# Kernel optimization log

Hardware: AMD Instinct MI355X
Metric: run time of the kernel (lower is better)

The kernel has to match this reference:

```python
import jax, jax.numpy as jnp
import numpy as np

B, L, DIN = 2, 4096, 1024
W = 64            # windowsize
G, H = 8, 8       # groups, heads per group
DQ = DV = 64
FF = 1024
NEG = -1e30


def rmsnorm(x, gamma, d):
    # F.normalize(x, dim=-1) * sqrt(d) * gamma
    n = jnp.sqrt(jnp.sum(x * x, axis=-1, keepdims=True))
    return x / jnp.maximum(n, 1e-12) * (d ** 0.5) * gamma


def setup_inputs() -> dict:
    key = jax.random.key(0)
    ks = jax.random.split(key, 8)
    s = 0.02
    return {
        "x": jax.random.normal(ks[0], (B, L, DIN), jnp.float32),
        "norm_gamma": jnp.ones((DIN,), jnp.float32),
        "Wq_w": jax.random.normal(ks[1], (G * H * DQ, DIN), jnp.float32) * s,
        "Wq_b": jnp.zeros((G * H * DQ,), jnp.float32),
        "Wkv_w": jax.random.normal(ks[2], (G * (DQ + DV), DIN), jnp.float32) * s,
        "Wkv_b": jnp.zeros((G * (DQ + DV),), jnp.float32),
        "wz_gamma1": jnp.ones((G * H * DV,), jnp.float32),
        "W1_w": jax.random.normal(ks[3], (2 * FF, G * H * DV), jnp.float32) * s,
        "W1_b": jnp.zeros((2 * FF,), jnp.float32),
        "wz_gamma2": jnp.ones((2 * FF,), jnp.float32),
        "W2_w": jax.random.normal(ks[4], (FF, 2 * FF), jnp.float32) * s,
        "W2_b": jnp.zeros((FF,), jnp.float32),
    }


def reference(x, norm_gamma, Wq_w, Wq_b, Wkv_w, Wkv_b,
              wz_gamma1, W1_w, W1_b, wz_gamma2, W2_w, W2_b):
    w2, w4 = W // 2, W // 4
    S = 2 * L // W  # number of query chunks (L % W == 0 -> drop_last path)

    xn = rmsnorm(x, norm_gamma, DIN)
    q = xn @ Wq_w.T + Wq_b          # [B, L, G*H*DQ]
    kv = xn @ Wkv_w.T + Wkv_b       # [B, L, G*(DQ+DV)]

    # pad_to_multiple(kv, W, mod=W//2): L % W == 0 -> append W//2 zeros
    kv = jnp.pad(kv, ((0, 0), (0, w2), (0, 0)))
    k, v = jnp.split(kv, 2, axis=-1)  # each [B, L+W/2, G*DQ]
    # F.pad W//4 both sides, then overlapping windows of size W, stride W//2
    k = jnp.pad(k, ((0, 0), (w4, w4), (0, 0)))  # [B, L+W, G*DQ]
    v = jnp.pad(v, ((0, 0), (w4, w4), (0, 0)))
    idx = jnp.arange(S)[:, None] * w2 + jnp.arange(W)[None, :]  # [S, W] (drop_last applied)
    kwin = k[:, idx].reshape(B, S, W, G, DQ).transpose(0, 3, 1, 2, 4)  # [B,G,S,W,DQ]
    vwin = v[:, idx].reshape(B, S, W, G, DV).transpose(0, 3, 1, 2, 4)  # [B,G,S,W,DV]

    # 'B (S w) (G H D) -> B G H S w D'
    qh = q.reshape(B, S, w2, G, H, DQ).transpose(0, 3, 4, 1, 2, 5)  # [B,G,H,S,w2,DQ]

    qk = jnp.einsum('bghsqd,bgskd->bghsqk', qh, kwin) * (1.0 / DQ ** 0.5)
    # edge masking: first chunk can't see left pad, last chunk can't see right pad
    maskb = jnp.zeros((S, W), bool).at[0, :w4].set(True).at[S - 1, W - w4:].set(True)
    qk = jnp.where(maskb[None, None, None, :, None, :], NEG, qk)
    attn = jax.nn.softmax(qk, axis=-1)
    o = jnp.einsum('bghsqk,bgskd->bghsqd', attn, vwin)
    o = o.transpose(0, 3, 4, 1, 2, 5).reshape(B, L, G * H * DV)  # 'B G H S w D -> B (S w) (G H D)'

    # Wz: RMSNorm -> Linear -> SiLU -> RMSNorm -> Linear -> SiLU (dropout=0)
    z = rmsnorm(o, wz_gamma1, G * H * DV)
    z = jax.nn.silu(z @ W1_w.T + W1_b)
    z = rmsnorm(z, wz_gamma2, 2 * FF)
    z = jax.nn.silu(z @ W2_w.T + W2_b)
    return z
```

## Files before the change

kernel.cpp:

```cpp
#include <hip/hip_runtime.h>
#include <cstdint>

typedef _Float16 f16;
typedef f16 f16x4 __attribute__((ext_vector_type(4)));
typedef f16 f16x8 __attribute__((ext_vector_type(8)));
typedef float f32x4 __attribute__((ext_vector_type(4)));

#define MFMA16(a, b, c) __builtin_amdgcn_mfma_f32_16x16x32_f16(a, b, c, 0, 0, 0)

static __device__ __forceinline__ void gload16(const void* g, void* l) {
    __builtin_amdgcn_global_load_lds(
        (const __attribute__((address_space(1))) uint32_t*)g,
        (__attribute__((address_space(3))) uint32_t*)l, 16, 0, 0);
}

template <int NM, int ND, int NV>
static __device__ __forceinline__ void sgb_phase() {
    if (NV > 0) __builtin_amdgcn_sched_group_barrier(0x10, NV, 0);
    constexpr int PER = NM / ND;
#pragma unroll
    for (int i = 0; i < ND; ++i) {
        __builtin_amdgcn_sched_group_barrier(0x8, PER, 0);
        __builtin_amdgcn_sched_group_barrier(0x100, 1, 0);
    }
    if (NM - PER * ND > 0)
        __builtin_amdgcn_sched_group_barrier(0x8, NM - PER * ND, 0);
}

static __device__ __forceinline__ float blockReduceSum256(float v) {
    __shared__ float red[4];
#pragma unroll
    for (int off = 32; off > 0; off >>= 1) v += __shfl_xor(v, off);
    if ((threadIdx.x & 63) == 0) red[threadIdx.x >> 6] = v;
    __syncthreads();
    return red[0] + red[1] + red[2] + red[3];
}

__global__ __launch_bounds__(256) void k_rmsnorm_x(const float* __restrict__ x,
                                                   const float* __restrict__ gamma,
                                                   f16* __restrict__ out) {
    size_t row = blockIdx.x;
    const float4 v = reinterpret_cast<const float4*>(x + row * 1024)[threadIdx.x];
    float ss = v.x * v.x + v.y * v.y + v.z * v.z + v.w * v.w;
    ss = blockReduceSum256(ss);
    float sc = 32.0f / fmaxf(sqrtf(ss), 1e-12f);
    const float4 g = reinterpret_cast<const float4*>(gamma)[threadIdx.x];
    f16x4 o;
    o[0] = (f16)(v.x * sc * g.x); o[1] = (f16)(v.y * sc * g.y);
    o[2] = (f16)(v.z * sc * g.z); o[3] = (f16)(v.w * sc * g.w);
    *reinterpret_cast<f16x4*>(out + row * 1024 + threadIdx.x * 4) = o;
}

__global__ __launch_bounds__(256) void k_prep(
    const float* __restrict__ Wq_w, const float* __restrict__ Wkv_w,
    const float* __restrict__ W1_w, const float* __restrict__ g1,
    const float* __restrict__ W2_w, const float* __restrict__ g2,
    const float* __restrict__ Wq_b, const float* __restrict__ Wkv_b,
    f16* __restrict__ wqkv, f16* __restrict__ w1, f16* __restrict__ w2,
    float* __restrict__ cb, float* __restrict__ scz) {
    int i = blockIdx.x * 256 + threadIdx.x;
    if (i < 1048576) {
        float4 v = reinterpret_cast<const float4*>(Wq_w)[i];
        f16x4 o; o[0] = (f16)v.x; o[1] = (f16)v.y; o[2] = (f16)v.z; o[3] = (f16)v.w;
        *reinterpret_cast<f16x4*>(wqkv + (size_t)i * 4) = o;
    } else if (i < 1310720) {
        int j = i - 1048576;
        float4 v = reinterpret_cast<const float4*>(Wkv_w)[j];
        f16x4 o; o[0] = (f16)v.x; o[1] = (f16)v.y; o[2] = (f16)v.z; o[3] = (f16)v.w;
        *reinterpret_cast<f16x4*>(wqkv + 4194304 + (size_t)j * 4) = o;
    } else if (i < 3407872) {
        int j = i - 1310720;
        float4 v = reinterpret_cast<const float4*>(W1_w)[j];
        int c = (j * 4) & 4095;
        f16x4 o;
        o[0] = (f16)(v.x * g1[c]);     o[1] = (f16)(v.y * g1[c + 1]);
        o[2] = (f16)(v.z * g1[c + 2]); o[3] = (f16)(v.w * g1[c + 3]);
        *reinterpret_cast<f16x4*>(w1 + (size_t)j * 4) = o;
    } else if (i < 3932160) {
        int j = i - 3407872;
        float4 v = reinterpret_cast<const float4*>(W2_w)[j];
        int c = (j * 4) & 2047;
        f16x4 o;
        o[0] = (f16)(v.x * g2[c]);     o[1] = (f16)(v.y * g2[c + 1]);
        o[2] = (f16)(v.z * g2[c + 2]); o[3] = (f16)(v.w * g2[c + 3]);
        *reinterpret_cast<f16x4*>(w2 + (size_t)j * 4) = o;
    } else if (i < 3933440) {
        int j = i - 3932160;
        int e = j * 4;
        float4 o4 = (e < 4096) ? reinterpret_cast<const float4*>(Wq_b)[j]
                               : reinterpret_cast<const float4*>(Wkv_b)[(e - 4096) >> 2];
        reinterpret_cast<float4*>(cb)[j] = o4;
    } else if (i < 3937536) {
        int j = i - 3933440;
        reinterpret_cast<float4*>(scz)[j] = make_float4(0.f, 0.f, 0.f, 0.f);
    }
}

template <int BN, int EPI, int MODE>
__global__ __launch_bounds__(512, 2) void k_gemm8p(const f16* __restrict__ A,
                                                   const f16* __restrict__ Bt,
                                                   const float* __restrict__ bias,
                                                   const float* __restrict__ ssin,
                                                   float sqrtD,
                                                   float* __restrict__ ssout,
                                                   void* __restrict__ Cout,
                                                   int M, int N, int K) {
    constexpr int BM = 256;
    constexpr int WN = BN / 64, WM = 8 / WN, WR = BM / WM;
    constexpr int MW = WR / 16, MH = MW / 2;
    constexpr int LA = 2, LB = BN / 128;
    constexpr int VS = 2 * LA + LB;
    constexpr int AK = BM * 32;
    constexpr int BKE = BN * 32;
    constexpr int SE = 2 * AK + 2 * BKE;

    __shared__ alignas(16) f16 lds[2 * SE];

    const int nb = N / BN;
    int bn, bm;
    if (MODE == 0) { bn = blockIdx.x & 7; bm = blockIdx.x >> 3; }
    else           { bn = blockIdx.x % nb; bm = blockIdx.x / nb; }

    const int tid = threadIdx.x, w = tid >> 6, l = tid & 63;
    const int wm = w / WN, wn = w % WN;
    const int lrow = l & 15, lq = l >> 4;
    const int g = (lrow >> 1) & 3;

    const f16* Ab = A + (size_t)bm * BM * K;
    const f16* Bb = Bt + (size_t)bn * BN * K;
    const int NT = K >> 6;

    int aoff[MW], boff[4];
#pragma unroll
    for (int m = 0; m < MW; ++m)
        aoff[m] = (wm * WR + m * 16 + lrow) * 32 + 8 * (lq ^ g);
#pragma unroll
    for (int n = 0; n < 4; ++n)
        boff[n] = (wn * 64 + n * 16 + lrow) * 32 + 8 * (lq ^ g);

    auto stageA = [&](int k0, f16* region) {
#pragma unroll
        for (int q = 0; q < LA; ++q) {
            int r = q * 128 + w * 16 + (l >> 2);
            int c = 8 * ((l & 3) ^ ((r >> 1) & 3));
            gload16(Ab + (size_t)r * K + k0 + c, region + q * 4096 + w * 512);
        }
    };
    auto stageB = [&](int k0, f16* region) {
#pragma unroll
        for (int q = 0; q < LB; ++q) {
            int r = q * 128 + w * 16 + (l >> 2);
            int c = 8 * ((l & 3) ^ ((r >> 1) & 3));
            gload16(Bb + (size_t)r * K + k0 + c, region + q * 4096 + w * 512);
        }
    };
    auto rdA = [&](f16x8 (&d)[MH], const f16* base, int h) {
#pragma unroll
        for (int m = 0; m < MH; ++m)
            d[m] = *reinterpret_cast<const f16x8*>(base + aoff[h * MH + m]);
    };
    auto rdB = [&](f16x8 (&d)[4], const f16* base) {
#pragma unroll
        for (int n = 0; n < 4; ++n)
            d[n] = *reinterpret_cast<const f16x8*>(base + boff[n]);
    };

    f32x4 acc[MW][4] = {};
    f16x8 afA[MH], afB[MH], bfA[4], bfB[4];

    auto mfmaLo = [&](f16x8 (&af)[MH], f16x8 (&bf)[4]) {
#pragma unroll
        for (int m = 0; m < MH; ++m)
#pragma unroll
            for (int n = 0; n < 4; ++n)
                acc[m][n] = MFMA16(af[m], bf[n], acc[m][n]);
    };
    auto mfmaHi = [&](f16x8 (&af)[MH], f16x8 (&bf)[4]) {
#pragma unroll
        for (int m = 0; m < MH; ++m)
#pragma unroll
            for (int n = 0; n < 4; ++n)
                acc[MH + m][n] = MFMA16(af[m], bf[n], acc[MH + m][n]);
    };

    stageA(0, lds);             stageB(0, lds + 2 * AK);
    stageA(32, lds + AK);       stageB(32, lds + 2 * AK + BKE);
    stageA(64, lds + SE);       stageB(64, lds + SE + 2 * AK);
    asm volatile("s_waitcnt vmcnt(%0)" :: "i"(2 * (LA + LB)) : "memory");
    __builtin_amdgcn_s_barrier();
    rdA(afA, lds, 0);
    rdB(bfA, lds + 2 * AK);

    const int NTm2 = NT - 2;
    for (int t = 0; t < NTm2; ++t) {
        f16* s0 = lds + (t & 1) * SE;
        f16* s1 = lds + ((t & 1) ^ 1) * SE;
        const int kn1 = (t + 1) << 6;
        const int kn2 = (t + 2) << 6;
        __builtin_amdgcn_s_barrier();
        stageA(kn1 + 32, s1 + AK);
        rdA(afB, s0, 1);
        mfmaLo(afA, bfA);
        sgb_phase<MH * 4, MH, LA>();
        asm volatile("s_waitcnt vmcnt(%0)" :: "i"(VS) : "memory");
        __builtin_amdgcn_s_barrier();
        stageB(kn1 + 32, s1 + 2 * AK + BKE);
        rdA(afA, s0 + AK, 0);
        rdB(bfB, s0 + 2 * AK + BKE);
        mfmaHi(afB, bfA);
        sgb_phase<MH * 4, MH + 4, LB>();
        __builtin_amdgcn_s_barrier();
        stageA(kn2, s0);
        rdA(afB, s0 + AK, 1);
        mfmaLo(afA, bfB);
        sgb_phase<MH * 4, MH, LA>();
        asm volatile("s_waitcnt vmcnt(%0)" :: "i"(VS) : "memory");
        __builtin_amdgcn_s_barrier();
        stageB(kn2, s0 + 2 * AK);
        rdA(afA, s1, 0);
        rdB(bfA, s1 + 2 * AK);
        mfmaHi(afB, bfB);
        sgb_phase<MH * 4, MH + 4, LB>();
    }
    {
        const int t = NTm2;
        f16* s0 = lds + (t & 1) * SE;
        f16* s1 = lds + ((t & 1) ^ 1) * SE;
        const int kn1 = (t + 1) << 6;
        __builtin_amdgcn_s_barrier();
        stageA(kn1 + 32, s1 + AK);
        rdA(afB, s0, 1);
        mfmaLo(afA, bfA);
        sgb_phase<MH * 4, MH, LA>();
        asm volatile("s_waitcnt vmcnt(%0)" :: "i"(VS) : "memory");
        __builtin_amdgcn_s_barrier();
        stageB(kn1 + 32, s1 + 2 * AK + BKE);
        rdA(afA, s0 + AK, 0);
        rdB(bfB, s0 + 2 * AK + BKE);
        mfmaHi(afB, bfA);
        sgb_phase<MH * 4, MH + 4, LB>();
        __builtin_amdgcn_s_barrier();
        rdA(afB, s0 + AK, 1);
        mfmaLo(afA, bfB);
        sgb_phase<MH * 4, MH, 0>();
        asm volatile("s_waitcnt vmcnt(%0)" :: "i"(LA + LB) : "memory");
        __builtin_amdgcn_s_barrier();
        rdA(afA, s1, 0);
        rdB(bfA, s1 + 2 * AK);
        mfmaHi(afB, bfB);
        sgb_phase<MH * 4, MH + 4, 0>();
    }
    {
        f16* s0 = lds + ((NT - 1) & 1) * SE;
        __builtin_amdgcn_s_barrier();
        rdA(afB, s0, 1);
        mfmaLo(afA, bfA);
        sgb_phase<MH * 4, MH, 0>();
        asm volatile("s_waitcnt vmcnt(0)" ::: "memory");
        __builtin_amdgcn_s_barrier();
        rdA(afA, s0 + AK, 0);
        rdB(bfB, s0 + 2 * AK + BKE);
        mfmaHi(afB, bfA);
        sgb_phase<MH * 4, MH + 4, 0>();
        __builtin_amdgcn_s_barrier();
        rdA(afB, s0 + AK, 1);
        mfmaLo(afA, bfB);
        sgb_phase<MH * 4, MH, 0>();
        mfmaHi(afB, bfB);
    }

    const size_t row0 = (size_t)bm * BM + wm * WR;
    const int col0 = bn * BN + wn * 64;
    float bsv[4];
#pragma unroll
    for (int n = 0; n < 4; ++n) bsv[n] = bias[col0 + n * 16 + lrow];
#pragma unroll
    for (int m = 0; m < MW; ++m) {
#pragma unroll
        for (int r = 0; r < 4; ++r) {
            const size_t row = row0 + m * 16 + lq * 4 + r;
            float scl = 1.0f;
            if (EPI >= 1)
                scl = sqrtD / fmaxf(sqrtf(ssin[row]), 1e-12f);
            float ssp = 0.f;
#pragma unroll
            for (int n = 0; n < 4; ++n) {
                float v = acc[m][n][r];
                if (EPI >= 1) v = v * scl;
                v += bsv[n];
                if (EPI >= 1) v = v / (1.f + __expf(-v));
                if (EPI == 1) ssp += v * v;
                const size_t idx = row * N + col0 + n * 16 + lrow;
                if (EPI == 2) reinterpret_cast<float*>(Cout)[idx] = v;
                else          reinterpret_cast<f16*>(Cout)[idx] = (f16)v;
            }
            if (EPI == 1) {
                ssp += __shfl_xor(ssp, 1);
                ssp += __shfl_xor(ssp, 2);
                ssp += __shfl_xor(ssp, 4);
                ssp += __shfl_xor(ssp, 8);
                if (lrow == 0) atomicAdd(&ssout[row], ssp);
            }
        }
    }
}

__global__ __launch_bounds__(256) void k_attn(const f16* __restrict__ qkv,
                                              f16* __restrict__ o,
                                              float* __restrict__ ssout) {
    __shared__ alignas(16) f16 Ksm[64 * 64];
    __shared__ alignas(16) f16 Vtsm[64 * 64];
    __shared__ alignas(16) f16 Psm[4][64 * 64];
    const int idx = blockIdx.x;
    const int s = idx & 127;
    const int g = (idx >> 7) & 7;
    const int b = idx >> 10;
    const int tid = threadIdx.x;
    const int w = tid >> 6, l = tid & 63;

    const int baseR = s * 32 - 16;
#pragma unroll
    for (int i = 0; i < 2; ++i) {
        const int j = i * 32 + (tid >> 3);
        const int d0 = (tid & 7) * 8;
        const int R = baseR + j;
        f16x8 kvv = {}, vvv = {};
        if (R >= 0 && R < 4096) {
            const f16* rp = qkv + ((size_t)(b * 4096 + R)) * 5120 + 4096 + g * 64 + d0;
            kvv = *reinterpret_cast<const f16x8*>(rp);
            vvv = *reinterpret_cast<const f16x8*>(rp + 512);
        }
        *reinterpret_cast<f16x8*>(&Ksm[j * 64 + d0]) = kvv;
#pragma unroll
        for (int e = 0; e < 8; ++e) Vtsm[(d0 + e) * 64 + j] = vvv[e];
    }

    const int lrow = l & 15, lk = (l >> 4) * 8;
    f16x8 aq[4][2];
#pragma unroll
    for (int m = 0; m < 4; ++m) {
        const int qr = w * 64 + m * 16 + lrow;
        const int h = qr >> 5, qi = qr & 31;
        const f16* qp = qkv + ((size_t)(b * 4096 + s * 32 + qi)) * 5120 + (g * 8 + h) * 64 + lk;
        aq[m][0] = *reinterpret_cast<const f16x8*>(qp);
        aq[m][1] = *reinterpret_cast<const f16x8*>(qp + 32);
    }
    __syncthreads();

    f32x4 acc[4][4] = {};
#pragma unroll
    for (int kk = 0; kk < 2; ++kk) {
        f16x8 bk[4];
#pragma unroll
        for (int n = 0; n < 4; ++n)
            bk[n] = *reinterpret_cast<const f16x8*>(&Ksm[(n * 16 + lrow) * 64 + kk * 32 + lk]);
#pragma unroll
        for (int m = 0; m < 4; ++m)
#pragma unroll
            for (int n = 0; n < 4; ++n)
                acc[m][n] = MFMA16(aq[m][kk], bk[n], acc[m][n]);
    }

    const int nlo = (s == 0) ? 1 : 0;
    const int nhi = (s == 127) ? 3 : 4;
#pragma unroll
    for (int m = 0; m < 4; ++m) {
#pragma unroll
        for (int r = 0; r < 4; ++r) {
            float xv[4];
#pragma unroll
            for (int n = 0; n < 4; ++n) xv[n] = acc[m][n][r] * 0.125f;
            float mx = -1e30f;
            for (int n = nlo; n < nhi; ++n) mx = fmaxf(mx, xv[n]);
#pragma unroll
            for (int off = 8; off > 0; off >>= 1) mx = fmaxf(mx, __shfl_xor(mx, off));
            float pv[4]; float sum = 0.f;
#pragma unroll
            for (int n = 0; n < 4; ++n) {
                float e = (n >= nlo && n < nhi) ? __expf(xv[n] - mx) : 0.f;
                pv[n] = e; sum += e;
            }
#pragma unroll
            for (int off = 8; off > 0; off >>= 1) sum += __shfl_xor(sum, off);
            const float inv = 1.f / sum;
            const int prow = m * 16 + (l >> 4) * 4 + r;
#pragma unroll
            for (int n = 0; n < 4; ++n)
                Psm[w][prow * 64 + n * 16 + lrow] = (f16)(pv[n] * inv);
        }
    }
    __syncthreads();

    f32x4 oacc[4][4] = {};
#pragma unroll
    for (int kk = 0; kk < 2; ++kk) {
        f16x8 ap[4], bv[4];
#pragma unroll
        for (int m = 0; m < 4; ++m)
            ap[m] = *reinterpret_cast<const f16x8*>(&Psm[w][(m * 16 + lrow) * 64 + kk * 32 + lk]);
#pragma unroll
        for (int n = 0; n < 4; ++n)
            bv[n] = *reinterpret_cast<const f16x8*>(&Vtsm[(n * 16 + lrow) * 64 + kk * 32 + lk]);
#pragma unroll
        for (int m = 0; m < 4; ++m)
#pragma unroll
            for (int n = 0; n < 4; ++n)
                oacc[m][n] = MFMA16(ap[m], bv[n], oacc[m][n]);
    }
    const int lr4 = (l >> 4) * 4;
#pragma unroll
    for (int m = 0; m < 4; ++m) {
#pragma unroll
        for (int r = 0; r < 4; ++r) {
            const int qr = w * 64 + m * 16 + lr4 + r;
            const int h = qr >> 5, qi = qr & 31;
            f16* op = o + ((size_t)(b * 4096 + s * 32 + qi)) * 4096 + (g * 8 + h) * 64;
            float ssp = 0.f;
#pragma unroll
            for (int n = 0; n < 4; ++n) {
                float v = oacc[m][n][r];
                op[n * 16 + lrow] = (f16)v;
                ssp += v * v;
            }
            ssp += __shfl_xor(ssp, 1);
            ssp += __shfl_xor(ssp, 2);
            ssp += __shfl_xor(ssp, 4);
            ssp += __shfl_xor(ssp, 8);
            if (lrow == 0)
                atomicAdd(&ssout[(size_t)(b * 4096 + s * 32 + qi)], ssp);
        }
    }
}

extern "C" void kernel_launch(void* const* d_in, const int* in_sizes, int n_in,
                              void* d_out, int out_size, void* d_ws, size_t ws_size,
                              hipStream_t stream) {
    const float* x     = (const float*)d_in[0];
    const float* ng    = (const float*)d_in[1];
    const float* Wq_w  = (const float*)d_in[2];
    const float* Wq_b  = (const float*)d_in[3];
    const float* Wkv_w = (const float*)d_in[4];
    const float* Wkv_b = (const float*)d_in[5];
    const float* g1    = (const float*)d_in[6];
    const float* W1_w  = (const float*)d_in[7];
    const float* W1_b  = (const float*)d_in[8];
    const float* g2    = (const float*)d_in[9];
    const float* W2_w  = (const float*)d_in[10];
    const float* W2_b  = (const float*)d_in[11];
    float* out = (float*)d_out;

    char* p = (char*)d_ws;
    f16* qkv  = (f16*)(p);
    f16* h1   = (f16*)(p);
    f16* xn   = (f16*)(p + 83886080);
    f16* ob   = (f16*)(p + 83886080);
    f16* w1   = (f16*)(p + 150994944);
    f16* w2   = (f16*)(p + 167772160);
    f16* wqkv = (f16*)(p + 171966464);
    float* cb  = (float*)(p + 182452224);
    float* sc1 = (float*)(p + 182472704);
    float* sc2 = (float*)(p + 182505472);

    k_prep<<<15381, 256, 0, stream>>>(Wq_w, Wkv_w, W1_w, g1, W2_w, g2, Wq_b, Wkv_b,
                                      wqkv, w1, w2, cb, sc1);
    k_rmsnorm_x<<<8192, 256, 0, stream>>>(x, ng, xn);

    k_gemm8p<256, 0, 1><<<640, 512, 0, stream>>>(xn, wqkv, cb, nullptr, 0.f, nullptr,
                                                 qkv, 8192, 5120, 1024);

    k_attn<<<2048, 256, 0, stream>>>(qkv, ob, sc1);

    k_gemm8p<256, 1, 0><<<256, 512, 0, stream>>>(ob, w1, W1_b, sc1, 64.0f, sc2,
                                                 h1, 8192, 2048, 4096);
    k_gemm8p<128, 2, 0><<<256, 512, 0, stream>>>(h1, w2, W2_b, sc2, 45.254834f, nullptr,
                                                 (void*)out, 8192, 1024, 2048);

    (void)in_sizes; (void)n_in; (void)out_size; (void)ws_size;
}
```

Before: 370.2 us.

## Switch GEMMs to 32x32x16 MFMA with XCD-aware tiling and separate row-norm pass

Replaces the 16x16x32 MFMA GEMM with a 32x32x16 variant that reads both A and B fragments per half-K step and uses wider accumulator tiles. It also adds an XCD-aware block-to-tile mapping so that blocks on the same XCD share A rows. The atomic sum-of-squares in the W1 epilogue is dropped, and a separate row reduction kernel over h1 now produces the norms for the W2 GEMM. The aim is higher MFMA throughput and fewer LDS reads per flop, at the cost of an extra launch that rereads h1 and higher register pressure.

Result: no change. 366.7 us (-1.0%).

```diff
diff --git a/kernel.cpp b/kernel.cpp
--- a/kernel.cpp
+++ b/kernel.cpp
@@ -5,8 +5,10 @@
 typedef f16 f16x4 __attribute__((ext_vector_type(4)));
 typedef f16 f16x8 __attribute__((ext_vector_type(8)));
 typedef float f32x4 __attribute__((ext_vector_type(4)));
+typedef float f32x16 __attribute__((ext_vector_type(16)));
 
 #define MFMA16(a, b, c) __builtin_amdgcn_mfma_f32_16x16x32_f16(a, b, c, 0, 0, 0)
+#define MFMA32(a, b, c) __builtin_amdgcn_mfma_f32_32x32x16_f16(a, b, c, 0, 0, 0)
 
 static __device__ __forceinline__ void gload16(const void* g, void* l) {
     __builtin_amdgcn_global_load_lds(
@@ -49,6 +51,24 @@
     o[0] = (f16)(v.x * sc * g.x); o[1] = (f16)(v.y * sc * g.y);
     o[2] = (f16)(v.z * sc * g.z); o[3] = (f16)(v.w * sc * g.w);
     *reinterpret_cast<f16x4*>(out + row * 1024 + threadIdx.x * 4) = o;
+}
+
+template <int D>
+__global__ __launch_bounds__(256) void k_rowss(const f16* __restrict__ in,
+                                               float* __restrict__ sc) {
+    constexpr int PER = D / 256;
+    size_t row = blockIdx.x;
+    const f16* ir = in + row * D;
+    int c0 = threadIdx.x * PER;
+    float ss = 0.f;
+#pragma unroll
+    for (int i = 0; i < PER; i += 8) {
+        f16x8 h = *reinterpret_cast<const f16x8*>(ir + c0 + i);
+#pragma unroll
+        for (int e = 0; e < 8; ++e) { float f = (float)h[e]; ss += f * f; }
+    }
+    ss = blockReduceSum256(ss);
+    if (threadIdx.x == 0) sc[row] = ss;
 }
 
 __global__ __launch_bounds__(256) void k_prep(
@@ -96,47 +116,55 @@
     }
 }
 
-template <int BN, int EPI, int MODE>
-__global__ __launch_bounds__(512, 2) void k_gemm8p(const f16* __restrict__ A,
+template <int BN, int EPI>
+__global__ __launch_bounds__(512, 2) void k_gemm32(const f16* __restrict__ A,
                                                    const f16* __restrict__ Bt,
                                                    const float* __restrict__ bias,
                                                    const float* __restrict__ ssin,
                                                    float sqrtD,
-                                                   float* __restrict__ ssout,
                                                    void* __restrict__ Cout,
                                                    int M, int N, int K) {
     constexpr int BM = 256;
-    constexpr int WN = BN / 64, WM = 8 / WN, WR = BM / WM;
-    constexpr int MW = WR / 16, MH = MW / 2;
+    constexpr int WN = BN / 64, WM = 8 / WN;
+    constexpr int WR = BM / WM, WC = BN / WN;
+    constexpr int MA = WR / 32, NB = WC / 32;
     constexpr int LA = 2, LB = BN / 128;
     constexpr int VS = 2 * LA + LB;
-    constexpr int AK = BM * 32;
-    constexpr int BKE = BN * 32;
+    constexpr int AK = BM * 32, BKE = BN * 32;
     constexpr int SE = 2 * AK + 2 * BKE;
 
     __shared__ alignas(16) f16 lds[2 * SE];
 
-    const int nb = N / BN;
-    int bn, bm;
-    if (MODE == 0) { bn = blockIdx.x & 7; bm = blockIdx.x >> 3; }
-    else           { bn = blockIdx.x % nb; bm = blockIdx.x / nb; }
+    const int mb = M / BM;
+    const int cpx = mb >> 3;
+    const int xcd = blockIdx.x & 7;
+    const int j = blockIdx.x >> 3;
+    const int bm = xcd * cpx + (j % cpx);
+    const int bn = j / cpx;
 
     const int tid = threadIdx.x, w = tid >> 6, l = tid & 63;
     const int wm = w / WN, wn = w % WN;
-    const int lrow = l & 15, lq = l >> 4;
-    const int g = (lrow >> 1) & 3;
+    const int cl = l & 31, h = l >> 5;
 
     const f16* Ab = A + (size_t)bm * BM * K;
     const f16* Bb = Bt + (size_t)bn * BN * K;
     const int NT = K >> 6;
 
-    int aoff[MW], boff[4];
-#pragma unroll
-    for (int m = 0; m < MW; ++m)
-        aoff[m] = (wm * WR + m * 16 + lrow) * 32 + 8 * (lq ^ g);
-#pragma unroll
-    for (int n = 0; n < 4; ++n)
-        boff[n] = (wn * 64 + n * 16 + lrow) * 32 + 8 * (lq ^ g);
+    int aoff[MA][2], boff[NB][2];
+#pragma unroll
+    for (int m = 0; m < MA; ++m) {
+        int r = wm * WR + m * 32 + cl;
+        int gg = (r >> 1) & 3;
+        aoff[m][0] = r * 32 + 8 * (h ^ gg);
+        aoff[m][1] = r * 32 + 8 * ((2 | h) ^ gg);
+    }
+#pragma unroll
+    for (int n = 0; n < NB; ++n) {
+        int r = wn * WC + n * 32 + cl;
+        int gg = (r >> 1) & 3;
+        boff[n][0] = r * 32 + 8 * (h ^ gg);
+        boff[n][1] = r * 32 + 8 * ((2 | h) ^ gg);
+    }
 
     auto stageA = [&](int k0, f16* region) {
 #pragma unroll
@@ -154,33 +182,26 @@
             gload16(Bb + (size_t)r * K + k0 + c, region + q * 4096 + w * 512);
         }
     };
-    auto rdA = [&](f16x8 (&d)[MH], const f16* base, int h) {
-#pragma unroll
-        for (int m = 0; m < MH; ++m)
-            d[m] = *reinterpret_cast<const f16x8*>(base + aoff[h * MH + m]);
+
+    f32x16 acc[MA][NB] = {};
+    f16x8 afA[MA], afB[MA], bfA[NB], bfB[NB];
+
+    auto rdA = [&](f16x8 (&d)[MA], const f16* base, int p) {
+#pragma unroll
+        for (int m = 0; m < MA; ++m)
+            d[m] = *reinterpret_cast<const f16x8*>(base + aoff[m][p]);
     };
-    auto rdB = [&](f16x8 (&d)[4], const f16* base) {
-#pragma unroll
-        for (int n = 0; n < 4; ++n)
-            d[n] = *reinterpret_cast<const f16x8*>(base + boff[n]);
+    auto rdB = [&](f16x8 (&d)[NB], const f16* base, int p) {
+#pragma unroll
+        for (int n = 0; n < NB; ++n)
+            d[n] = *reinterpret_cast<const f16x8*>(base + boff[n][p]);
     };
-
-    f32x4 acc[MW][4] = {};
-    f16x8 afA[MH], afB[MH], bfA[4], bfB[4];
-
-    auto mfmaLo = [&](f16x8 (&af)[MH], f16x8 (&bf)[4]) {
-#pragma unroll
-        for (int m = 0; m < MH; ++m)
-#pragma unroll
-            for (int n = 0; n < 4; ++n)
-                acc[m][n] = MFMA16(af[m], bf[n], acc[m][n]);
-    };
-    auto mfmaHi = [&](f16x8 (&af)[MH], f16x8 (&bf)[4]) {
-#pragma unroll
-        for (int m = 0; m < MH; ++m)
-#pragma unroll
-            for (int n = 0; n < 4; ++n)
-                acc[MH + m][n] = MFMA16(af[m], bf[n], acc[MH + m][n]);
+    auto domfma = [&](f16x8 (&af)[MA], f16x8 (&bf)[NB]) {
+#pragma unroll
+        for (int m = 0; m < MA; ++m)
+#pragma unroll
+            for (int n = 0; n < NB; ++n)
+                acc[m][n] = MFMA32(af[m], bf[n], acc[m][n]);
     };
 
     stageA(0, lds);             stageB(0, lds + 2 * AK);
@@ -189,117 +210,100 @@
     asm volatile("s_waitcnt vmcnt(%0)" :: "i"(2 * (LA + LB)) : "memory");
     __builtin_amdgcn_s_barrier();
     rdA(afA, lds, 0);
-    rdB(bfA, lds + 2 * AK);
-
-    const int NTm2 = NT - 2;
-    for (int t = 0; t < NTm2; ++t) {
+    rdB(bfA, lds + 2 * AK, 0);
+
+    for (int t = 0; t < NT - 2; ++t) {
         f16* s0 = lds + (t & 1) * SE;
         f16* s1 = lds + ((t & 1) ^ 1) * SE;
         const int kn1 = (t + 1) << 6;
         const int kn2 = (t + 2) << 6;
         __builtin_amdgcn_s_barrier();
         stageA(kn1 + 32, s1 + AK);
-        rdA(afB, s0, 1);
-        mfmaLo(afA, bfA);
-        sgb_phase<MH * 4, MH, LA>();
+        rdA(afB, s0, 1); rdB(bfB, s0 + 2 * AK, 1);
+        domfma(afA, bfA);
+        sgb_phase<MA * NB, MA + NB, LA>();
         asm volatile("s_waitcnt vmcnt(%0)" :: "i"(VS) : "memory");
         __builtin_amdgcn_s_barrier();
         stageB(kn1 + 32, s1 + 2 * AK + BKE);
-        rdA(afA, s0 + AK, 0);
-        rdB(bfB, s0 + 2 * AK + BKE);
-        mfmaHi(afB, bfA);
-        sgb_phase<MH * 4, MH + 4, LB>();
+        rdA(afA, s0 + AK, 0); rdB(bfA, s0 + 2 * AK + BKE, 0);
+        domfma(afB, bfB);
+        sgb_phase<MA * NB, MA + NB, LB>();
         __builtin_amdgcn_s_barrier();
         stageA(kn2, s0);
-        rdA(afB, s0 + AK, 1);
-        mfmaLo(afA, bfB);
-        sgb_phase<MH * 4, MH, LA>();
+        rdA(afB, s0 + AK, 1); rdB(bfB, s0 + 2 * AK + BKE, 1);
+        domfma(afA, bfA);
+        sgb_phase<MA * NB, MA + NB, LA>();
         asm volatile("s_waitcnt vmcnt(%0)" :: "i"(VS) : "memory");
         __builtin_amdgcn_s_barrier();
         stageB(kn2, s0 + 2 * AK);
-        rdA(afA, s1, 0);
-        rdB(bfA, s1 + 2 * AK);
-        mfmaHi(afB, bfB);
-        sgb_phase<MH * 4, MH + 4, LB>();
+        rdA(afA, s1, 0); rdB(bfA, s1 + 2 * AK, 0);
+        domfma(afB, bfB);
+        sgb_phase<MA * NB, MA + NB, LB>();
     }
     {
-        const int t = NTm2;
+        const int t = NT - 2;
         f16* s0 = lds + (t & 1) * SE;
         f16* s1 = lds + ((t & 1) ^ 1) * SE;
         const int kn1 = (t + 1) << 6;
         __builtin_amdgcn_s_barrier();
         stageA(kn1 + 32, s1 + AK);
-        rdA(afB, s0, 1);
-        mfmaLo(afA, bfA);
-        sgb_phase<MH * 4, MH, LA>();
+        rdA(afB, s0, 1); rdB(bfB, s0 + 2 * AK, 1);
+        domfma(afA, bfA);
+        sgb_phase<MA * NB, MA + NB, LA>();
         asm volatile("s_waitcnt vmcnt(%0)" :: "i"(VS) : "memory");
         __builtin_amdgcn_s_barrier();
         stageB(kn1 + 32, s1 + 2 * AK + BKE);
-        rdA(afA, s0 + AK, 0);
-        rdB(bfB, s0 + 2 * AK + BKE);
-        mfmaHi(afB, bfA);
-        sgb_phase<MH * 4, MH + 4, LB>();
-        __builtin_amdgcn_s_barrier();
-        rdA(afB, s0 + AK, 1);
-        mfmaLo(afA, bfB);
-        sgb_phase<MH * 4, MH, 0>();
+        rdA(afA, s0 + AK, 0); rdB(bfA, s0 + 2 * AK + BKE, 0);
+        domfma(afB, bfB);
+        sgb_phase<MA * NB, MA + NB, LB>();
+        __builtin_amdgcn_s_barrier();
+        rdA(afB, s0 + AK, 1); rdB(bfB, s0 + 2 * AK + BKE, 1);
+        domfma(afA, bfA);
+        sgb_phase<MA * NB, MA + NB, 0>();
         asm volatile("s_waitcnt vmcnt(%0)" :: "i"(LA + LB) : "memory");
         __builtin_amdgcn_s_barrier();
-        rdA(afA, s1, 0);
-        rdB(bfA, s1 + 2 * AK);
-        mfmaHi(afB, bfB);
-        sgb_phase<MH * 4, MH + 4, 0>();
+        rdA(afA, s1, 0); rdB(bfA, s1 + 2 * AK, 0);
+        domfma(afB, bfB);
+        sgb_phase<MA * NB, MA + NB, 0>();
     }
     {
         f16* s0 = lds + ((NT - 1) & 1) * SE;
         __builtin_amdgcn_s_barrier();
-        rdA(afB, s0, 1);
-        mfmaLo(afA, bfA);
-        sgb_phase<MH * 4, MH, 0>();
+        rdA(afB, s0, 1); rdB(bfB, s0 + 2 * AK, 1);
+        domfma(afA, bfA);
+        sgb_phase<MA * NB, MA + NB, 0>();
         asm volatile("s_waitcnt vmcnt(0)" ::: "memory");
         __builtin_amdgcn_s_barrier();
-        rdA(afA, s0 + AK, 0);
-        rdB(bfB, s0 + 2 * AK + BKE);
-        mfmaHi(afB, bfA);
-        sgb_phase<MH * 4, MH + 4, 0>();
-        __builtin_amdgcn_s_barrier();
-        rdA(afB, s0 + AK, 1);
-        mfmaLo(afA, bfB);
-        sgb_phase<MH * 4, MH, 0>();
-        mfmaHi(afB, bfB);
+        rdA(afA, s0 + AK, 0); rdB(bfA, s0 + 2 * AK + BKE, 0);
+        domfma(afB, bfB);
+        sgb_phase<MA * NB, MA + NB, 0>();
+        rdA(afB, s0 + AK, 1); rdB(bfB, s0 + 2 * AK + BKE, 1);
+        domfma(afA, bfA);
+        sgb_phase<MA * NB, MA + NB, 0>();
+        domfma(afB, bfB);
     }
 
     const size_t row0 = (size_t)bm * BM + wm * WR;
-    const int col0 = bn * BN + wn * 64;
-    float bsv[4];
-#pragma unroll
-    for (int n = 0; n < 4; ++n) bsv[n] = bias[col0 + n * 16 + lrow];
-#pragma unroll
-    for (int m = 0; m < MW; ++m) {
-#pragma unroll
-        for (int r = 0; r < 4; ++r) {
-            const size_t row = row0 + m * 16 + lq * 4 + r;
+    const int col0 = bn * BN + wn * WC;
+    float bsv[NB];
+#pragma unroll
+    for (int n = 0; n < NB; ++n) bsv[n] = bias[col0 + n * 32 + cl];
+#pragma unroll
+    for (int m = 0; m < MA; ++m) {
+#pragma unroll
+        for (int jr = 0; jr < 16; ++jr) {
+            const size_t row = row0 + m * 32 + h * 4 + (jr & 3) + 8 * (jr >> 2);
             float scl = 1.0f;
-            if (EPI >= 1)
-                scl = sqrtD / fmaxf(sqrtf(ssin[row]), 1e-12f);
-            float ssp = 0.f;
-#pragma unroll
-            for (int n = 0; n < 4; ++n) {
-                float v = acc[m][n][r];
+            if (EPI >= 1) scl = sqrtD * rsqrtf(fmaxf(ssin[row], 1e-24f));
+#pragma unroll
+            for (int n = 0; n < NB; ++n) {
+                float v = acc[m][n][jr];
                 if (EPI >= 1) v = v * scl;
                 v += bsv[n];
                 if (EPI >= 1) v = v / (1.f + __expf(-v));
-                if (EPI == 1) ssp += v * v;
-                const size_t idx = row * N + col0 + n * 16 + lrow;
+                const size_t idx = row * (size_t)N + col0 + n * 32 + cl;
                 if (EPI == 2) reinterpret_cast<float*>(Cout)[idx] = v;
                 else          reinterpret_cast<f16*>(Cout)[idx] = (f16)v;
-            }
-            if (EPI == 1) {
-                ssp += __shfl_xor(ssp, 1);
-                ssp += __shfl_xor(ssp, 2);
-                ssp += __shfl_xor(ssp, 4);
-                ssp += __shfl_xor(ssp, 8);
-                if (lrow == 0) atomicAdd(&ssout[row], ssp);
             }
         }
     }
@@ -465,15 +469,16 @@
                                       wqkv, w1, w2, cb, sc1);
     k_rmsnorm_x<<<8192, 256, 0, stream>>>(x, ng, xn);
 
-    k_gemm8p<256, 0, 1><<<640, 512, 0, stream>>>(xn, wqkv, cb, nullptr, 0.f, nullptr,
-                                                 qkv, 8192, 5120, 1024);
+    k_gemm32<256, 0><<<640, 512, 0, stream>>>(xn, wqkv, cb, nullptr, 0.f,
+                                              qkv, 8192, 5120, 1024);
 
     k_attn<<<2048, 256, 0, stream>>>(qkv, ob, sc1);
 
-    k_gemm8p<256, 1, 0><<<256, 512, 0, stream>>>(ob, w1, W1_b, sc1, 64.0f, sc2,
-                                                 h1, 8192, 2048, 4096);
-    k_gemm8p<128, 2, 0><<<256, 512, 0, stream>>>(h1, w2, W2_b, sc2, 45.254834f, nullptr,
-                                                 (void*)out, 8192, 1024, 2048);
+    k_gemm32<256, 1><<<256, 512, 0, stream>>>(ob, w1, W1_b, sc1, 64.0f,
+                                              h1, 8192, 2048, 4096);
+    k_rowss<2048><<<8192, 256, 0, stream>>>(h1, sc2);
+    k_gemm32<128, 2><<<256, 512, 0, stream>>>(h1, w2, W2_b, sc2, 45.254834f,
+                                              (void*)out, 8192, 1024, 2048);
 
     (void)in_sizes; (void)n_in; (void)out_size; (void)ws_size;
 }
```

## Fuse x-rmsnorm into prep, move h1 sum-of-squares out of GEMM, remap tiles per XCD

Applied to the files above, without the earlier changes.

The input rmsnorm is merged into the weight-prep kernel, which saves one launch. The per-row sum of squares for the second norm is no longer built with atomics in the W1 GEMM epilogue. A separate k_rowss kernel now recomputes it from the stored f16 h1, which costs an extra read of h1. The GEMM block-to-tile mapping changes so that each XCD handles a contiguous band of M tiles, aiming at better L2 reuse. Computing the norm from f16 values instead of fp32 slightly changes precision.

Measured after the change: 345.8 us. -6.6%, faster.

```diff
diff --git a/kernel.cpp b/kernel.cpp
--- a/kernel.cpp
+++ b/kernel.cpp
@@ -36,29 +36,46 @@
     return red[0] + red[1] + red[2] + red[3];
 }
 
-__global__ __launch_bounds__(256) void k_rmsnorm_x(const float* __restrict__ x,
-                                                   const float* __restrict__ gamma,
-                                                   f16* __restrict__ out) {
+template <int D>
+__global__ __launch_bounds__(256) void k_rowss(const f16* __restrict__ in,
+                                               float* __restrict__ sc) {
+    constexpr int PER = D / 256;
     size_t row = blockIdx.x;
-    const float4 v = reinterpret_cast<const float4*>(x + row * 1024)[threadIdx.x];
-    float ss = v.x * v.x + v.y * v.y + v.z * v.z + v.w * v.w;
+    const f16* ir = in + row * D;
+    int c0 = threadIdx.x * PER;
+    float ss = 0.f;
+#pragma unroll
+    for (int i = 0; i < PER; i += 8) {
+        f16x8 h = *reinterpret_cast<const f16x8*>(ir + c0 + i);
+#pragma unroll
+        for (int e = 0; e < 8; ++e) { float f = (float)h[e]; ss += f * f; }
+    }
     ss = blockReduceSum256(ss);
-    float sc = 32.0f / fmaxf(sqrtf(ss), 1e-12f);
-    const float4 g = reinterpret_cast<const float4*>(gamma)[threadIdx.x];
-    f16x4 o;
-    o[0] = (f16)(v.x * sc * g.x); o[1] = (f16)(v.y * sc * g.y);
-    o[2] = (f16)(v.z * sc * g.z); o[3] = (f16)(v.w * sc * g.w);
-    *reinterpret_cast<f16x4*>(out + row * 1024 + threadIdx.x * 4) = o;
+    if (threadIdx.x == 0) sc[row] = ss;
 }
 
 __global__ __launch_bounds__(256) void k_prep(
+    const float* __restrict__ x, const float* __restrict__ ng, f16* __restrict__ xn,
     const float* __restrict__ Wq_w, const float* __restrict__ Wkv_w,
     const float* __restrict__ W1_w, const float* __restrict__ g1,
     const float* __restrict__ W2_w, const float* __restrict__ g2,
     const float* __restrict__ Wq_b, const float* __restrict__ Wkv_b,
     f16* __restrict__ wqkv, f16* __restrict__ w1, f16* __restrict__ w2,
     float* __restrict__ cb, float* __restrict__ scz) {
-    int i = blockIdx.x * 256 + threadIdx.x;
+    if (blockIdx.x < 8192) {
+        size_t row = blockIdx.x;
+        const float4 v = reinterpret_cast<const float4*>(x + row * 1024)[threadIdx.x];
+        float ss = v.x * v.x + v.y * v.y + v.z * v.z + v.w * v.w;
+        ss = blockReduceSum256(ss);
+        float sc = 32.0f / fmaxf(sqrtf(ss), 1e-12f);
+        const float4 g = reinterpret_cast<const float4*>(ng)[threadIdx.x];
+        f16x4 o;
+        o[0] = (f16)(v.x * sc * g.x); o[1] = (f16)(v.y * sc * g.y);
+        o[2] = (f16)(v.z * sc * g.z); o[3] = (f16)(v.w * sc * g.w);
+        *reinterpret_cast<f16x4*>(xn + row * 1024 + threadIdx.x * 4) = o;
+        return;
+    }
+    int i = (blockIdx.x - 8192) * 256 + threadIdx.x;
     if (i < 1048576) {
         float4 v = reinterpret_cast<const float4*>(Wq_w)[i];
         f16x4 o; o[0] = (f16)v.x; o[1] = (f16)v.y; o[2] = (f16)v.z; o[3] = (f16)v.w;
@@ -96,13 +113,12 @@
     }
 }
 
-template <int BN, int EPI, int MODE>
+template <int BN, int EPI>
 __global__ __launch_bounds__(512, 2) void k_gemm8p(const f16* __restrict__ A,
                                                    const f16* __restrict__ Bt,
                                                    const float* __restrict__ bias,
                                                    const float* __restrict__ ssin,
                                                    float sqrtD,
-                                                   float* __restrict__ ssout,
                                                    void* __restrict__ Cout,
                                                    int M, int N, int K) {
     constexpr int BM = 256;
@@ -116,10 +132,12 @@
 
     __shared__ alignas(16) f16 lds[2 * SE];
 
-    const int nb = N / BN;
-    int bn, bm;
-    if (MODE == 0) { bn = blockIdx.x & 7; bm = blockIdx.x >> 3; }
-    else           { bn = blockIdx.x % nb; bm = blockIdx.x / nb; }
+    const int mb = M / BM;
+    const int cpx = mb >> 3;
+    const int xcd = blockIdx.x & 7;
+    const int j = blockIdx.x >> 3;
+    const int bm = xcd * cpx + (j % cpx);
+    const int bn = j / cpx;
 
     const int tid = threadIdx.x, w = tid >> 6, l = tid & 63;
     const int wm = w / WN, wn = w % WN;
@@ -280,26 +298,16 @@
         for (int r = 0; r < 4; ++r) {
             const size_t row = row0 + m * 16 + lq * 4 + r;
             float scl = 1.0f;
-            if (EPI >= 1)
-                scl = sqrtD / fmaxf(sqrtf(ssin[row]), 1e-12f);
-            float ssp = 0.f;
+            if (EPI >= 1) scl = sqrtD * rsqrtf(fmaxf(ssin[row], 1e-24f));
 #pragma unroll
             for (int n = 0; n < 4; ++n) {
                 float v = acc[m][n][r];
                 if (EPI >= 1) v = v * scl;
                 v += bsv[n];
                 if (EPI >= 1) v = v / (1.f + __expf(-v));
-                if (EPI == 1) ssp += v * v;
-                const size_t idx = row * N + col0 + n * 16 + lrow;
+                const size_t idx = row * (size_t)N + col0 + n * 16 + lrow;
                 if (EPI == 2) reinterpret_cast<float*>(Cout)[idx] = v;
                 else          reinterpret_cast<f16*>(Cout)[idx] = (f16)v;
-            }
-            if (EPI == 1) {
-                ssp += __shfl_xor(ssp, 1);
-                ssp += __shfl_xor(ssp, 2);
-                ssp += __shfl_xor(ssp, 4);
-                ssp += __shfl_xor(ssp, 8);
-                if (lrow == 0) atomicAdd(&ssout[row], ssp);
             }
         }
     }
@@ -461,19 +469,20 @@
     float* sc1 = (float*)(p + 182472704);
     float* sc2 = (float*)(p + 182505472);
 
-    k_prep<<<15381, 256, 0, stream>>>(Wq_w, Wkv_w, W1_w, g1, W2_w, g2, Wq_b, Wkv_b,
-                                      wqkv, w1, w2, cb, sc1);
-    k_rmsnorm_x<<<8192, 256, 0, stream>>>(x, ng, xn);
-
-    k_gemm8p<256, 0, 1><<<640, 512, 0, stream>>>(xn, wqkv, cb, nullptr, 0.f, nullptr,
-                                                 qkv, 8192, 5120, 1024);
+    k_prep<<<8192 + 15381, 256, 0, stream>>>(x, ng, xn,
+                                             Wq_w, Wkv_w, W1_w, g1, W2_w, g2,
+                                             Wq_b, Wkv_b, wqkv, w1, w2, cb, sc1);
+
+    k_gemm8p<256, 0><<<640, 512, 0, stream>>>(xn, wqkv, cb, nullptr, 0.f,
+                                              qkv, 8192, 5120, 1024);
 
     k_attn<<<2048, 256, 0, stream>>>(qkv, ob, sc1);
 
-    k_gemm8p<256, 1, 0><<<256, 512, 0, stream>>>(ob, w1, W1_b, sc1, 64.0f, sc2,
-                                                 h1, 8192, 2048, 4096);
-    k_gemm8p<128, 2, 0><<<256, 512, 0, stream>>>(h1, w2, W2_b, sc2, 45.254834f, nullptr,
-                                                 (void*)out, 8192, 1024, 2048);
+    k_gemm8p<256, 1><<<256, 512, 0, stream>>>(ob, w1, W1_b, sc1, 64.0f,
+                                              h1, 8192, 2048, 4096);
+    k_rowss<2048><<<8192, 256, 0, stream>>>(h1, sc2);
+    k_gemm8p<128, 2><<<256, 512, 0, stream>>>(h1, w2, W2_b, sc2, 45.254834f,
+                                              (void*)out, 8192, 1024, 2048);
 
     (void)in_sizes; (void)n_in; (void)out_size; (void)ws_size;
 }
```
